# Kernel tuning notes

Hardware: AMD Instinct MI355X
Metric: run time of the kernel (lower is better)

## Reference

```python
import jax, jax.numpy as jnp
import numpy as np

NUM_HEADS = 4
EPS = 1e-5

def _proj(x, W, b):
    # 1x1x1 Conv3d == channel-wise linear: x [B,C,H,W,D], W [Cout,Cin], b [Cout]
    return jnp.einsum('oc,bchwd->bohwd', W, x) + b[None, :, None, None, None]

def setup_inputs() -> dict:
    key = jax.random.key(0)
    ks = jax.random.split(key, 12)
    B, C, H, W, D = 2, 128, 16, 16, 16
    s = 1.0 / np.sqrt(C)
    inp = {
        'query_features': jax.random.normal(ks[0], (B, C, H, W, D), jnp.float32),
        'key_value_features': jax.random.normal(ks[1], (B, C, H, W, D), jnp.float32),
        'Wq': jax.random.normal(ks[2], (C, C), jnp.float32) * s,
        'bq': jax.random.normal(ks[3], (C,), jnp.float32) * 0.01,
        'Wk': jax.random.normal(ks[4], (C, C), jnp.float32) * s,
        'bk': jax.random.normal(ks[5], (C,), jnp.float32) * 0.01,
        'Wv': jax.random.normal(ks[6], (C, C), jnp.float32) * s,
        'bv': jax.random.normal(ks[7], (C,), jnp.float32) * 0.01,
        'Wo': jax.random.normal(ks[8], (C, C), jnp.float32) * s,
        'bo': jax.random.normal(ks[9], (C,), jnp.float32) * 0.01,
    }
    return inp

def reference(query_features, key_value_features, Wq, bq, Wk, bk, Wv, bv, Wo, bo):
    B, C, H, W, D = query_features.shape
    hd = C // NUM_HEADS  # head_dim
    N = H * W * D
    Q = _proj(query_features, Wq, bq).reshape(B, NUM_HEADS, hd, N)
    K = _proj(key_value_features, Wk, bk).reshape(B, NUM_HEADS, hd, N)
    V = _proj(key_value_features, Wv, bv).reshape(B, NUM_HEADS, hd, N)
    scale = hd ** -0.5
    attn = jnp.einsum('bhdn,bhdm->bhnm', Q, K) * scale  # [B,h,N,N]
    attn = jax.nn.softmax(attn, axis=-1)
    out = jnp.einsum('bhnm,bhdm->bhdn', attn, V).reshape(B, C, H, W, D)
    out = _proj(out, Wo, bo)
    res = query_features + out
    # InstanceNorm3d (affine=False): normalize over spatial dims per (B,C)
    mu = jnp.mean(res, axis=(2, 3, 4), keepdims=True)
    var = jnp.var(res, axis=(2, 3, 4), keepdims=True)
    return (res - mu) * jax.lax.rsqrt(var + EPS)
```

## Files before the change

kernel.cpp:

```cpp
#include <hip/hip_runtime.h>
#include <hip/hip_bf16.h>

typedef unsigned short u16;
typedef unsigned int u32;
typedef __bf16 bf16_t;
typedef bf16_t bf16x8 __attribute__((ext_vector_type(8)));
typedef float f32x4 __attribute__((ext_vector_type(4)));

#define NTOT 4096
#define CCH 128
#define QSCL 0.25503486703f

__device__ __forceinline__ float bf2f(u16 x) {
    return __uint_as_float(((u32)x) << 16);
}
__device__ __forceinline__ u32 pkbf(float a, float b) {
    __hip_bfloat162 h = __float22bfloat162_rn(make_float2(a, b));
    u32 r; __builtin_memcpy(&r, &h, 4); return r;
}
__device__ __forceinline__ u16 f2bf(float a) {
    return (u16)(pkbf(a, a) & 0xffffu);
}

__global__ __launch_bounds__(256, 4) void proj_kernel(
    const float* __restrict__ xq, const float* __restrict__ xkv,
    const float* __restrict__ Wq, const float* __restrict__ bq,
    const float* __restrict__ Wk, const float* __restrict__ bk_,
    const float* __restrict__ Wv, const float* __restrict__ bv_,
    u16* __restrict__ Qt, u16* __restrict__ Kt, u16* __restrict__ Vn)
{
    const int nt = blockIdx.x, p = blockIdx.y, b = blockIdx.z;
    const float* X    = (p == 0) ? xq : xkv;
    const float* Wf   = (p == 0) ? Wq : (p == 1) ? Wk : Wv;
    const float* bias = (p == 0) ? bq : (p == 1) ? bk_ : bv_;
    const float s = (p == 0) ? QSCL : 1.0f;
    const int n0 = nt * 64;
    const int tid = threadIdx.x;

    __shared__ u16 Xt[64 * 128];
    __shared__ u16 Wl[128 * 136];

    #pragma unroll
    for (int k = 0; k < 4; ++k) {
        int n = tid & 63;
        int c = (tid >> 6) + k * 4;
        float f[8];
        #pragma unroll
        for (int j = 0; j < 8; ++j)
            f[j] = X[((size_t)(b * CCH) + 8 * c + j) * NTOT + n0 + n];
        uint4 vv = {pkbf(f[0], f[1]), pkbf(f[2], f[3]), pkbf(f[4], f[5]), pkbf(f[6], f[7])};
        *(uint4*)(Xt + n * 128 + ((c ^ (n & 7)) * 8)) = vv;
    }
    #pragma unroll
    for (int k = 0; k < 8; ++k) {
        int id = tid + k * 256;
        int row = id >> 4;
        int off = (id & 15) * 8;
        const float* wsrc = Wf + row * 128 + off;
        float4 wa = *(const float4*)(wsrc);
        float4 wc = *(const float4*)(wsrc + 4);
        uint4 vv = {pkbf(wa.x * s, wa.y * s), pkbf(wa.z * s, wa.w * s),
                    pkbf(wc.x * s, wc.y * s), pkbf(wc.z * s, wc.w * s)};
        *(uint4*)(Wl + row * 136 + off) = vv;
    }
    __syncthreads();

    const int wave = tid >> 6, lane = tid & 63;
    const int quad = lane >> 4, l16 = lane & 15;
    f32x4 acc[8];
    #pragma unroll
    for (int cf = 0; cf < 8; ++cf) acc[cf] = (f32x4){0.f, 0.f, 0.f, 0.f};

    #pragma unroll
    for (int kk = 0; kk < 4; ++kk) {
        bf16x8 bx = *(const bf16x8*)(Xt + (wave * 16 + l16) * 128 +
                                     (((kk * 4 + quad) ^ (l16 & 7)) * 8));
        #pragma unroll
        for (int cf = 0; cf < 8; ++cf) {
            bf16x8 aw = *(const bf16x8*)(Wl + (cf * 16 + l16) * 136 + kk * 32 + quad * 8);
            acc[cf] = __builtin_amdgcn_mfma_f32_16x16x32_bf16(aw, bx, acc[cf], 0, 0, 0);
        }
    }

    const int n = n0 + wave * 16 + l16;
    #pragma unroll
    for (int cf = 0; cf < 8; ++cf) {
        float4 b4 = *(const float4*)(bias + cf * 16 + quad * 4);
        float v0 = acc[cf][0] + b4.x * s;
        float v1 = acc[cf][1] + b4.y * s;
        float v2 = acc[cf][2] + b4.z * s;
        float v3 = acc[cf][3] + b4.w * s;
        if (p < 2) {
            const int h = cf >> 1;
            const int d0 = (cf & 1) * 16 + quad * 4;
            u16* dst = (p == 0 ? Qt : Kt) + ((size_t)(b * 4 + h) * NTOT + n) * 32 + d0;
            uint2 vv = {pkbf(v0, v1), pkbf(v2, v3)};
            *(uint2*)dst = vv;
        } else {
            int c = cf * 16 + quad * 4;
            u16* dst = Vn + (size_t)(b * CCH + c) * NTOT + n;
            dst[0 * NTOT] = f2bf(v0); dst[1 * NTOT] = f2bf(v1);
            dst[2 * NTOT] = f2bf(v2); dst[3 * NTOT] = f2bf(v3);
        }
    }
}

__global__ __launch_bounds__(256, 2) void flash_attn_kernel(
    const u16* __restrict__ Qt, const u16* __restrict__ Kt,
    const u16* __restrict__ Vn, u16* __restrict__ pO, float* __restrict__ pL)
{
    const int bh = blockIdx.z, kc = blockIdx.y;
    const int wave = threadIdx.x >> 6, lane = threadIdx.x & 63;
    const int q = lane >> 4, l16 = lane & 15;
    const int q0w = blockIdx.x * 256 + wave * 64;

    const u16* Qbh = Qt + (size_t)bh * NTOT * 32;
    const u16* Kbh = Kt + (size_t)bh * NTOT * 32;
    const u16* Vg  = Vn + ((size_t)((bh >> 2) * CCH + (bh & 3) * 32)) * NTOT;

    __shared__ u16 Ksh[8 * 2048];
    __shared__ u16 Vsh[8 * 2048];

    const int kbase = kc * 1024;

    bf16x8 bq[4];
    #pragma unroll
    for (int g = 0; g < 4; ++g)
        bq[g] = *(const bf16x8*)(Qbh + (size_t)(q0w + g * 16 + l16) * 32 + q * 8);

    bf16x8 aone;
    {
        u32 oo = 0x3F803F80u;
        uint4 uo = {oo, oo, oo, oo};
        __builtin_memcpy(&aone, &uo, 16);
    }

    const size_t kst0 = (size_t)(kbase + wave * 16 + l16) * 32 + q * 8;
    const size_t vst0 = (size_t)((wave & 1) * 16 + l16) * NTOT + kbase +
                        (wave >> 1) * 32 + q * 8;
    const int kds = wave * 512 + lane * 8;
    const int vds = wave * 512 + (q & 1) * 256 + l16 * 8 + (q >> 1) * 4;
    const int frd = lane * 8;

    f32x4 o[4][2];
    f32x4 ol[4];
    #pragma unroll
    for (int g = 0; g < 4; ++g) {
        o[g][0] = (f32x4){0,0,0,0};
        o[g][1] = (f32x4){0,0,0,0};
        ol[g]   = (f32x4){0,0,0,0};
    }
    const f32x4 zero = {0,0,0,0};

    for (int half = 0; half < 2; ++half) {
        if (half)
            __syncthreads();
        {
            const size_t kst = kst0 + (size_t)(half * 512) * 32;
            const size_t vst = vst0 + half * 512;
            #pragma unroll
            for (int m = 0; m < 8; ++m) {
                uint4 kr = *(const uint4*)(Kbh + kst + m * 2048);
                uint4 vr = *(const uint4*)(Vg + vst + m * 64);
                *(uint4*)(&Ksh[m * 2048 + kds]) = kr;
                uint2 va = {vr.x, vr.y};
                uint2 vb = {vr.z, vr.w};
                *(uint2*)(&Vsh[m * 2048 + vds])       = va;
                *(uint2*)(&Vsh[m * 2048 + vds + 128]) = vb;
            }
        }
        __syncthreads();

        bf16x8 ak[4], av[4];
        #pragma unroll
        for (int t = 0; t < 4; ++t) {
            ak[t] = *(const bf16x8*)(&Ksh[t * 512 + frd]);
            av[t] = *(const bf16x8*)(&Vsh[t * 512 + frd]);
        }

        for (int m = 0; m < 8; ++m) {
            bf16x8 nak[4], nav[4];
            if (m < 7) {
                const int nb = (m + 1) * 2048;
                #pragma unroll
                for (int t = 0; t < 4; ++t) {
                    nak[t] = *(const bf16x8*)(&Ksh[nb + t * 512 + frd]);
                    nav[t] = *(const bf16x8*)(&Vsh[nb + t * 512 + frd]);
                }
            }
            f32x4 s[4][4];
            #pragma unroll
            for (int t = 0; t < 4; ++t) {
                #pragma unroll
                for (int g = 0; g < 4; ++g)
                    s[g][t] = __builtin_amdgcn_mfma_f32_16x16x32_bf16(ak[t], bq[g], zero, 0, 0, 0);
            }
            #pragma unroll
            for (int g = 0; g < 4; ++g) {
                float e[4][4];
                #pragma unroll
                for (int t = 0; t < 4; ++t) {
                    e[t][0] = __builtin_amdgcn_exp2f(s[g][t][0]);
                    e[t][1] = __builtin_amdgcn_exp2f(s[g][t][1]);
                    e[t][2] = __builtin_amdgcn_exp2f(s[g][t][2]);
                    e[t][3] = __builtin_amdgcn_exp2f(s[g][t][3]);
                }
                uint4 u0 = {pkbf(e[0][0], e[0][1]), pkbf(e[0][2], e[0][3]),
                            pkbf(e[1][0], e[1][1]), pkbf(e[1][2], e[1][3])};
                uint4 u1 = {pkbf(e[2][0], e[2][1]), pkbf(e[2][2], e[2][3]),
                            pkbf(e[3][0], e[3][1]), pkbf(e[3][2], e[3][3])};
                bf16x8 pb0, pb1;
                __builtin_memcpy(&pb0, &u0, 16);
                __builtin_memcpy(&pb1, &u1, 16);
                o[g][0] = __builtin_amdgcn_mfma_f32_16x16x32_bf16(av[0], pb0, o[g][0], 0, 0, 0);
                o[g][1] = __builtin_amdgcn_mfma_f32_16x16x32_bf16(av[1], pb0, o[g][1], 0, 0, 0);
                o[g][0] = __builtin_amdgcn_mfma_f32_16x16x32_bf16(av[2], pb1, o[g][0], 0, 0, 0);
                o[g][1] = __builtin_amdgcn_mfma_f32_16x16x32_bf16(av[3], pb1, o[g][1], 0, 0, 0);
                ol[g]   = __builtin_amdgcn_mfma_f32_16x16x32_bf16(aone,  pb0, ol[g],   0, 0, 0);
                ol[g]   = __builtin_amdgcn_mfma_f32_16x16x32_bf16(aone,  pb1, ol[g],   0, 0, 0);
            }
            if (m < 7) {
                #pragma unroll
                for (int t = 0; t < 4; ++t) { ak[t] = nak[t]; av[t] = nav[t]; }
            }
        }
    }

    #pragma unroll
    for (int g = 0; g < 4; ++g) {
        const size_t ob = ((size_t)(kc * 8 + bh) * NTOT + q0w + g * 16 + l16) * 32 + q * 4;
        uint2 w0 = {pkbf(o[g][0][0], o[g][0][1]), pkbf(o[g][0][2], o[g][0][3])};
        uint2 w1 = {pkbf(o[g][1][0], o[g][1][1]), pkbf(o[g][1][2], o[g][1][3])};
        *(uint2*)(pO + ob)      = w0;
        *(uint2*)(pO + ob + 16) = w1;
        if (q == 0)
            pL[(size_t)(kc * 8 + bh) * NTOT + q0w + g * 16 + l16] = ol[g][0];
    }
}

__global__ __launch_bounds__(256, 4) void outproj_kernel(
    const float* __restrict__ xq,
    const u16* __restrict__ pO, const float* __restrict__ pL,
    const float* __restrict__ Wo, const float* __restrict__ bo,
    float* __restrict__ res, float* __restrict__ partS, float* __restrict__ partQ)
{
    const int nt = blockIdx.x, ct = blockIdx.y, b = blockIdx.z;
    const int n0 = nt * 32;
    const int tid = threadIdx.x;

    __shared__ u16 Xt[32 * 128];
    __shared__ u16 Wl[64 * 136];

    #pragma unroll
    for (int k = 0; k < 2; ++k) {
        int cid = tid + k * 256;
        int n = cid >> 4;
        int ch = cid & 15;
        int bh = b * 4 + (ch >> 2);
        int d0 = (ch & 3) * 8;
        float l = 0.f;
        float v[8];
        #pragma unroll
        for (int j = 0; j < 8; ++j) v[j] = 0.f;
        #pragma unroll
        for (int kcc = 0; kcc < 4; ++kcc) {
            const size_t nrow = (size_t)(kcc * 8 + bh) * NTOT + n0 + n;
            l += pL[nrow];
            uint4 u = *(const uint4*)(pO + nrow * 32 + d0);
            const u32 uu[4] = {u.x, u.y, u.z, u.w};
            #pragma unroll
            for (int j = 0; j < 4; ++j) {
                v[2 * j]     += bf2f((u16)(uu[j] & 0xffffu));
                v[2 * j + 1] += bf2f((u16)(uu[j] >> 16));
            }
        }
        const float inv = 1.0f / l;
        uint4 vv = {pkbf(v[0] * inv, v[1] * inv), pkbf(v[2] * inv, v[3] * inv),
                    pkbf(v[4] * inv, v[5] * inv), pkbf(v[6] * inv, v[7] * inv)};
        *(uint4*)(Xt + n * 128 + ((ch ^ (n & 7)) * 8)) = vv;
    }
    #pragma unroll
    for (int k = 0; k < 4; ++k) {
        int id = tid + k * 256;
        int row = id >> 4;
        int off = (id & 15) * 8;
        const float* wsrc = Wo + (size_t)(ct * 64 + row) * 128 + off;
        float4 wa = *(const float4*)(wsrc);
        float4 wc = *(const float4*)(wsrc + 4);
        uint4 vv = {pkbf(wa.x, wa.y), pkbf(wa.z, wa.w),
                    pkbf(wc.x, wc.y), pkbf(wc.z, wc.w)};
        *(uint4*)(Wl + row * 136 + off) = vv;
    }
    __syncthreads();

    const int wave = tid >> 6, lane = tid & 63;
    const int quad = lane >> 4, l16 = lane & 15;
    const int nh = wave & 1, chh = wave >> 1;
    f32x4 acc[2];
    #pragma unroll
    for (int cf = 0; cf < 2; ++cf) acc[cf] = (f32x4){0.f, 0.f, 0.f, 0.f};

    #pragma unroll
    for (int kk = 0; kk < 4; ++kk) {
        bf16x8 bx = *(const bf16x8*)(Xt + (nh * 16 + l16) * 128 +
                                     (((kk * 4 + quad) ^ (l16 & 7)) * 8));
        #pragma unroll
        for (int cf = 0; cf < 2; ++cf) {
            bf16x8 aw = *(const bf16x8*)(Wl + (chh * 32 + cf * 16 + l16) * 136 +
                                         kk * 32 + quad * 8);
            acc[cf] = __builtin_amdgcn_mfma_f32_16x16x32_bf16(aw, bx, acc[cf], 0, 0, 0);
        }
    }

    const int n = n0 + nh * 16 + l16;
    const int tile = nt * 2 + nh;
    #pragma unroll
    for (int cf = 0; cf < 2; ++cf) {
        const int cbase = ct * 64 + chh * 32 + cf * 16 + quad * 4;
        float4 b4 = *(const float4*)(bo + cbase);
        const float bb[4] = {b4.x, b4.y, b4.z, b4.w};
        float sv[4], qv[4];
        #pragma unroll
        for (int r = 0; r < 4; ++r) {
            int c = cbase + r;
            float v = acc[cf][r] + bb[r] + xq[(size_t)(b * CCH + c) * NTOT + n];
            res[(size_t)(b * CCH + c) * NTOT + n] = v;
            sv[r] = v;
            qv[r] = v * v;
        }
        #pragma unroll
        for (int off = 1; off < 16; off <<= 1) {
            #pragma unroll
            for (int r = 0; r < 4; ++r) {
                sv[r] += __shfl_xor(sv[r], off);
                qv[r] += __shfl_xor(qv[r], off);
            }
        }
        if (l16 == 0) {
            #pragma unroll
            for (int r = 0; r < 4; ++r) {
                int c = cbase + r;
                partS[(size_t)(b * CCH + c) * 256 + tile] = sv[r];
                partQ[(size_t)(b * CCH + c) * 256 + tile] = qv[r];
            }
        }
    }
}

__global__ __launch_bounds__(256) void norm_kernel(
    const float* __restrict__ res, const float* __restrict__ partS,
    const float* __restrict__ partQ, float* __restrict__ out)
{
    const int c = blockIdx.x, b = blockIdx.y, zq = blockIdx.z;
    const int tid = threadIdx.x;
    const size_t row = (size_t)(b * CCH + c);
    __shared__ float rs[4], rq[4];
    float s = partS[row * 256 + tid];
    float q = partQ[row * 256 + tid];
    #pragma unroll
    for (int off = 1; off < 64; off <<= 1) {
        s += __shfl_xor(s, off);
        q += __shfl_xor(q, off);
    }
    const int wv = tid >> 6, ln = tid & 63;
    if (ln == 0) { rs[wv] = s; rq[wv] = q; }
    __syncthreads();
    float ts = rs[0] + rs[1] + rs[2] + rs[3];
    float tq = rq[0] + rq[1] + rq[2] + rq[3];
    float mu  = ts * (1.0f / 4096.0f);
    float var = tq * (1.0f / 4096.0f) - mu * mu;
    float inv = rsqrtf(var + 1e-5f);
    const size_t base = row * NTOT;
    const int n = tid * 4 + zq * 1024;
    float4 v = *(const float4*)(res + base + n);
    float4 o;
    o.x = (v.x - mu) * inv; o.y = (v.y - mu) * inv;
    o.z = (v.z - mu) * inv; o.w = (v.w - mu) * inv;
    *(float4*)(out + base + n) = o;
}

extern "C" void kernel_launch(void* const* d_in, const int* in_sizes, int n_in,
                              void* d_out, int out_size, void* d_ws, size_t ws_size,
                              hipStream_t stream)
{
    const float* xq  = (const float*)d_in[0];
    const float* xkv = (const float*)d_in[1];
    const float* Wq  = (const float*)d_in[2];
    const float* bq  = (const float*)d_in[3];
    const float* Wk  = (const float*)d_in[4];
    const float* bk  = (const float*)d_in[5];
    const float* Wv  = (const float*)d_in[6];
    const float* bv  = (const float*)d_in[7];
    const float* Wo  = (const float*)d_in[8];
    const float* bo  = (const float*)d_in[9];
    float* out = (float*)d_out;

    char* ws = (char*)d_ws;
    const size_t MB = (size_t)1 << 20;
    u16* Qt = (u16*)(ws + 0 * MB);
    u16* Kt = (u16*)(ws + 2 * MB);
    u16* Vn = (u16*)(ws + 4 * MB);
    u16* pO = (u16*)(ws + 6 * MB);
    float* pL = (float*)(ws + 14 * MB);
    float* res   = (float*)(ws + 16 * MB);
    float* partS = (float*)(ws + 20 * MB);
    float* partQ = (float*)(ws + 20 * MB + 262144);

    proj_kernel<<<dim3(64, 3, 2), 256, 0, stream>>>(xq, xkv, Wq, bq, Wk, bk, Wv, bv, Qt, Kt, Vn);
    flash_attn_kernel<<<dim3(16, 4, 8), 256, 0, stream>>>(Qt, Kt, Vn, pO, pL);
    outproj_kernel<<<dim3(128, 2, 2), 256, 0, stream>>>(xq, pO, pL, Wo, bo, res, partS, partQ);
    norm_kernel<<<dim3(128, 2, 4), 256, 0, stream>>>(res, partS, partQ, out);
}
```

Before: 121.5 us.

## Split flash-attention blocks into 8 waves with 32 queries each and specialized loaders

Result: no change. 121.5 us (+0.0%).

```diff
diff --git a/kernel.cpp b/kernel.cpp
--- a/kernel.cpp
+++ b/kernel.cpp
@@ -105,14 +105,14 @@
     }
 }
 
-__global__ __launch_bounds__(256, 2) void flash_attn_kernel(
+__global__ __launch_bounds__(512, 4) void flash_attn_kernel(
     const u16* __restrict__ Qt, const u16* __restrict__ Kt,
     const u16* __restrict__ Vn, u16* __restrict__ pO, float* __restrict__ pL)
 {
     const int bh = blockIdx.z, kc = blockIdx.y;
     const int wave = threadIdx.x >> 6, lane = threadIdx.x & 63;
     const int q = lane >> 4, l16 = lane & 15;
-    const int q0w = blockIdx.x * 256 + wave * 64;
+    const int q0w = blockIdx.x * 256 + wave * 32;
 
     const u16* Qbh = Qt + (size_t)bh * NTOT * 32;
     const u16* Kbh = Kt + (size_t)bh * NTOT * 32;
@@ -123,9 +123,9 @@
 
     const int kbase = kc * 1024;
 
-    bf16x8 bq[4];
-    #pragma unroll
-    for (int g = 0; g < 4; ++g)
+    bf16x8 bq[2];
+    #pragma unroll
+    for (int g = 0; g < 2; ++g)
         bq[g] = *(const bf16x8*)(Qbh + (size_t)(q0w + g * 16 + l16) * 32 + q * 8);
 
     bf16x8 aone;
@@ -135,17 +135,18 @@
         __builtin_memcpy(&aone, &uo, 16);
     }
 
-    const size_t kst0 = (size_t)(kbase + wave * 16 + l16) * 32 + q * 8;
-    const size_t vst0 = (size_t)((wave & 1) * 16 + l16) * NTOT + kbase +
-                        (wave >> 1) * 32 + q * 8;
-    const int kds = wave * 512 + lane * 8;
-    const int vds = wave * 512 + (q & 1) * 256 + l16 * 8 + (q >> 1) * 4;
+    const int w4 = wave & 3;
+    const size_t kst0 = (size_t)(kbase + w4 * 16 + l16) * 32 + q * 8;
+    const size_t vst0 = (size_t)((w4 & 1) * 16 + l16) * NTOT + kbase +
+                        (w4 >> 1) * 32 + q * 8;
+    const int kds = w4 * 512 + lane * 8;
+    const int vds = w4 * 512 + (q & 1) * 256 + l16 * 8 + (q >> 1) * 4;
     const int frd = lane * 8;
 
-    f32x4 o[4][2];
-    f32x4 ol[4];
-    #pragma unroll
-    for (int g = 0; g < 4; ++g) {
+    f32x4 o[2][2];
+    f32x4 ol[2];
+    #pragma unroll
+    for (int g = 0; g < 2; ++g) {
         o[g][0] = (f32x4){0,0,0,0};
         o[g][1] = (f32x4){0,0,0,0};
         ol[g]   = (f32x4){0,0,0,0};
@@ -155,14 +156,18 @@
     for (int half = 0; half < 2; ++half) {
         if (half)
             __syncthreads();
-        {
+        if (wave < 4) {
             const size_t kst = kst0 + (size_t)(half * 512) * 32;
-            const size_t vst = vst0 + half * 512;
             #pragma unroll
             for (int m = 0; m < 8; ++m) {
                 uint4 kr = *(const uint4*)(Kbh + kst + m * 2048);
+                *(uint4*)(&Ksh[m * 2048 + kds]) = kr;
+            }
+        } else {
+            const size_t vst = vst0 + half * 512;
+            #pragma unroll
+            for (int m = 0; m < 8; ++m) {
                 uint4 vr = *(const uint4*)(Vg + vst + m * 64);
-                *(uint4*)(&Ksh[m * 2048 + kds]) = kr;
                 uint2 va = {vr.x, vr.y};
                 uint2 vb = {vr.z, vr.w};
                 *(uint2*)(&Vsh[m * 2048 + vds])       = va;
@@ -171,44 +176,35 @@
         }
         __syncthreads();
 
-        bf16x8 ak[4], av[4];
-        #pragma unroll
-        for (int t = 0; t < 4; ++t) {
-            ak[t] = *(const bf16x8*)(&Ksh[t * 512 + frd]);
-            av[t] = *(const bf16x8*)(&Vsh[t * 512 + frd]);
-        }
-
         for (int m = 0; m < 8; ++m) {
-            bf16x8 nak[4], nav[4];
-            if (m < 7) {
-                const int nb = (m + 1) * 2048;
+            const int mb = m * 2048;
+            bf16x8 ak[4], av[4];
+            #pragma unroll
+            for (int t = 0; t < 4; ++t) {
+                ak[t] = *(const bf16x8*)(&Ksh[mb + t * 512 + frd]);
+                av[t] = *(const bf16x8*)(&Vsh[mb + t * 512 + frd]);
+            }
+            f32x4 s[2][4];
+            #pragma unroll
+            for (int t = 0; t < 4; ++t) {
+                #pragma unroll
+                for (int g = 0; g < 2; ++g)
+                    s[g][t] = __builtin_amdgcn_mfma_f32_16x16x32_bf16(ak[t], bq[g], zero, 0, 0, 0);
+            }
+            #pragma unroll
+            for (int g = 0; g < 2; ++g) {
+                u32 uw[8];
                 #pragma unroll
                 for (int t = 0; t < 4; ++t) {
-                    nak[t] = *(const bf16x8*)(&Ksh[nb + t * 512 + frd]);
-                    nav[t] = *(const bf16x8*)(&Vsh[nb + t * 512 + frd]);
+                    float e0 = __builtin_amdgcn_exp2f(s[g][t][0]);
+                    float e1 = __builtin_amdgcn_exp2f(s[g][t][1]);
+                    float e2 = __builtin_amdgcn_exp2f(s[g][t][2]);
+                    float e3 = __builtin_amdgcn_exp2f(s[g][t][3]);
+                    uw[t * 2]     = pkbf(e0, e1);
+                    uw[t * 2 + 1] = pkbf(e2, e3);
                 }
-            }
-            f32x4 s[4][4];
-            #pragma unroll
-            for (int t = 0; t < 4; ++t) {
-                #pragma unroll
-                for (int g = 0; g < 4; ++g)
-                    s[g][t] = __builtin_amdgcn_mfma_f32_16x16x32_bf16(ak[t], bq[g], zero, 0, 0, 0);
-            }
-            #pragma unroll
-            for (int g = 0; g < 4; ++g) {
-                float e[4][4];
-                #pragma unroll
-                for (int t = 0; t < 4; ++t) {
-                    e[t][0] = __builtin_amdgcn_exp2f(s[g][t][0]);
-                    e[t][1] = __builtin_amdgcn_exp2f(s[g][t][1]);
-                    e[t][2] = __builtin_amdgcn_exp2f(s[g][t][2]);
-                    e[t][3] = __builtin_amdgcn_exp2f(s[g][t][3]);
-                }
-                uint4 u0 = {pkbf(e[0][0], e[0][1]), pkbf(e[0][2], e[0][3]),
-                            pkbf(e[1][0], e[1][1]), pkbf(e[1][2], e[1][3])};
-                uint4 u1 = {pkbf(e[2][0], e[2][1]), pkbf(e[2][2], e[2][3]),
-                            pkbf(e[3][0], e[3][1]), pkbf(e[3][2], e[3][3])};
+                uint4 u0 = {uw[0], uw[1], uw[2], uw[3]};
+                uint4 u1 = {uw[4], uw[5], uw[6], uw[7]};
                 bf16x8 pb0, pb1;
                 __builtin_memcpy(&pb0, &u0, 16);
                 __builtin_memcpy(&pb1, &u1, 16);
@@ -219,15 +215,11 @@
                 ol[g]   = __builtin_amdgcn_mfma_f32_16x16x32_bf16(aone,  pb0, ol[g],   0, 0, 0);
                 ol[g]   = __builtin_amdgcn_mfma_f32_16x16x32_bf16(aone,  pb1, ol[g],   0, 0, 0);
             }
-            if (m < 7) {
-                #pragma unroll
-                for (int t = 0; t < 4; ++t) { ak[t] = nak[t]; av[t] = nav[t]; }
-            }
-        }
-    }
-
-    #pragma unroll
-    for (int g = 0; g < 4; ++g) {
+        }
+    }
+
+    #pragma unroll
+    for (int g = 0; g < 2; ++g) {
         const size_t ob = ((size_t)(kc * 8 + bh) * NTOT + q0w + g * 16 + l16) * 32 + q * 4;
         uint2 w0 = {pkbf(o[g][0][0], o[g][0][1]), pkbf(o[g][0][2], o[g][0][3])};
         uint2 w1 = {pkbf(o[g][1][0], o[g][1][1]), pkbf(o[g][1][2], o[g][1][3])};
@@ -407,7 +399,7 @@
     float* partQ = (float*)(ws + 20 * MB + 262144);
 
     proj_kernel<<<dim3(64, 3, 2), 256, 0, stream>>>(xq, xkv, Wq, bq, Wk, bk, Wv, bv, Qt, Kt, Vn);
-    flash_attn_kernel<<<dim3(16, 4, 8), 256, 0, stream>>>(Qt, Kt, Vn, pO, pL);
+    flash_attn_kernel<<<dim3(16, 4, 8), 512, 0, stream>>>(Qt, Kt, Vn, pO, pL);
     outproj_kernel<<<dim3(128, 2, 2), 256, 0, stream>>>(xq, pO, pL, Wo, bo, res, partS, partQ);
     norm_kernel<<<dim3(128, 2, 4), 256, 0, stream>>>(res, partS, partQ, out);
 }
```
